# Kernel optimization log

Hardware: AMD Instinct MI355X
Metric: run time of the kernel (lower is better)

## Reference

```python
import jax, jax.numpy as jnp
import numpy as np

N = 100000
E = 1600000
D_IN = 128
HID = 128
N_CLASSES = 40
NEG_SLOPE = 0.2  # PyG GATConv default
BN_EPS = 1e-5


def setup_inputs() -> dict:
    key = jax.random.key(0)
    ks = jax.random.split(key, 16)
    s = 0.1
    return {
        "x": jax.random.normal(ks[0], (N, D_IN), dtype=jnp.float32),
        "edge_index": jax.random.randint(ks[1], (2, E), 0, N, dtype=jnp.int64),
        # GAT layer 1 (in=D_IN, out=HID, heads=1)
        "W1": jax.random.normal(ks[2], (D_IN, HID), dtype=jnp.float32) * s,
        "a_src1": jax.random.normal(ks[3], (HID,), dtype=jnp.float32) * s,
        "a_dst1": jax.random.normal(ks[4], (HID,), dtype=jnp.float32) * s,
        "b1": jnp.zeros((HID,), dtype=jnp.float32),
        # GAT layer 2 (in=HID, out=HID, heads=1)
        "W2": jax.random.normal(ks[5], (HID, HID), dtype=jnp.float32) * s,
        "a_src2": jax.random.normal(ks[6], (HID,), dtype=jnp.float32) * s,
        "a_dst2": jax.random.normal(ks[7], (HID,), dtype=jnp.float32) * s,
        "b2": jnp.zeros((HID,), dtype=jnp.float32),
        # shared BatchNorm1d(HID) applied after every conv
        "gamma": jnp.ones((HID,), dtype=jnp.float32),
        "beta": jnp.zeros((HID,), dtype=jnp.float32),
        # output Linear(HID, N_CLASSES)
        "Wout": jax.random.normal(ks[8], (HID, N_CLASSES), dtype=jnp.float32) * s,
        "bout": jnp.zeros((N_CLASSES,), dtype=jnp.float32),
    }


def reference(x, edge_index, W1, a_src1, a_dst1, b1, W2, a_src2, a_dst2, b2,
              gamma, beta, Wout, bout):
    n = x.shape[0]
    loops = jnp.arange(n, dtype=edge_index.dtype)  # add_self_loops (GATConv default)
    src = jnp.concatenate([edge_index[0], loops])
    dst = jnp.concatenate([edge_index[1], loops])

    def gat_layer(h_in, W, a_s, a_d, b):
        h = h_in @ W                                   # [N, HID]
        e_src = h @ a_s                                # [N] per-node src score
        e_dst = h @ a_d                                # [N] per-node dst score
        e = jax.nn.leaky_relu(e_src[src] + e_dst[dst], NEG_SLOPE)  # [E+N]
        # segment softmax over incoming edges of each dst node
        m = jax.ops.segment_max(e, dst, num_segments=n)
        p = jnp.exp(e - m[dst])
        denom = jax.ops.segment_sum(p, dst, num_segments=n)
        alpha = p / denom[dst]
        out = jax.ops.segment_sum(alpha[:, None] * h[src], dst, num_segments=n)
        return out + b

    def bn_elu(z):
        mu = z.mean(axis=0)
        var = ((z - mu) ** 2).mean(axis=0)  # biased var (BN training mode)
        zh = (z - mu) / jnp.sqrt(var + BN_EPS) * gamma + beta
        return jax.nn.elu(zh)

    h = bn_elu(gat_layer(x, W1, a_src1, a_dst1, b1))
    h = bn_elu(gat_layer(h, W2, a_src2, a_dst2, b2))
    return h @ Wout + bout
```

## Files before the change

kernel.cpp:

```cpp
#include <hip/hip_runtime.h>

#define NNODES 100000
#define NEDGES 1600000
#define ET (NEDGES + NNODES)
#define NBUCK 782
#define NEG 0.2f
#define BNEPS 1e-5f
#define EPB 4096
#define NBLK_E ((ET + EPB - 1) / EPB)

typedef __attribute__((ext_vector_type(8))) short short8;
typedef __attribute__((ext_vector_type(4))) float floatx4;
typedef __attribute__((ext_vector_type(2))) float floatx2;

__device__ __forceinline__ unsigned short f2b(float x) {
    unsigned int u = __float_as_uint(x);
    u += 0x7fff + ((u >> 16) & 1);
    return (unsigned short)(u >> 16);
}
__device__ __forceinline__ float b2f(unsigned short u) {
    return __uint_as_float(((unsigned int)u) << 16);
}
__device__ __forceinline__ float blo2f(unsigned int v) {
    return __uint_as_float(v << 16);
}
__device__ __forceinline__ float bhi2f(unsigned int v) {
    return __uint_as_float(v & 0xffff0000u);
}
__device__ __forceinline__ floatx2 u2f2(unsigned int v) {
    floatx2 r;
    r.x = __uint_as_float(v << 16);
    r.y = __uint_as_float(v & 0xffff0000u);
    return r;
}

__device__ __forceinline__ int edge_src(const int* ei, int e, int w64) {
    if (e >= NEDGES) return e - NEDGES;
    return w64 ? ei[2 * e] : ei[e];
}
__device__ __forceinline__ int edge_dst(const int* ei, int e, int w64) {
    if (e >= NEDGES) return e - NEDGES;
    return w64 ? ei[2 * (NEDGES + e)] : ei[NEDGES + e];
}

__global__ void k_prep(const float* __restrict__ W1, const float* __restrict__ W2,
                       unsigned short* __restrict__ WT1, unsigned short* __restrict__ WT2,
                       const int* ei, int* flag, int* bcnt, int* done, float* bnstat) {
    int t = blockIdx.x * 256 + threadIdx.x;
    if (t < 800) bcnt[t] = 0;
    if (blockIdx.x == 4) {
        bnstat[threadIdx.x] = 0.f;
    } else if (blockIdx.x == 5) {
        bnstat[256 + threadIdx.x] = 0.f;
    }
    if (t == 0) *done = 0;
    if (t == 1) {
        int is64 = 1;
        for (int j = 1; j < 16; j += 2)
            if (ei[j] != 0) is64 = 0;
        *flag = is64;
    }
    int k = t >> 7, n = t & 127;
    WT1[n * 128 + k] = f2b(W1[t]);
    WT2[n * 128 + k] = f2b(W2[t]);
}

__global__ __launch_bounds__(256) void k_bhist(const int* __restrict__ ei,
                                               const int* flag, int* bcnt,
                                               int* done, int* bbase, int* bcur) {
    __shared__ int lc[784];
    __shared__ int sh[256];
    __shared__ int lastf;
    int t = threadIdx.x;
    for (int i = t; i < NBUCK; i += 256) lc[i] = 0;
    __syncthreads();
    int w64 = *flag;
    int base = blockIdx.x * EPB;
    for (int j = 0; j < EPB / 512; j++) {
        int e = base + j * 512 + t * 2;
        if (e + 1 < NEDGES) {
            int d0, d1;
            if (w64) {
                int4 dv = *(const int4*)&ei[2 * (NEDGES + e)];
                d0 = dv.x; d1 = dv.z;
            } else {
                int2 dv = *(const int2*)&ei[NEDGES + e];
                d0 = dv.x; d1 = dv.y;
            }
            atomicAdd(&lc[d0 >> 7], 1);
            atomicAdd(&lc[d1 >> 7], 1);
        } else {
            for (int k = 0; k < 2; k++) {
                int ee = e + k;
                if (ee < ET) atomicAdd(&lc[edge_dst(ei, ee, w64) >> 7], 1);
            }
        }
    }
    __syncthreads();
    for (int i = t; i < NBUCK; i += 256)
        if (lc[i]) atomicAdd(&bcnt[i], lc[i]);
    __threadfence();
    __syncthreads();
    if (t == 0) lastf = (atomicAdd(done, 1) == gridDim.x - 1) ? 1 : 0;
    __syncthreads();
    if (!lastf) return;
    int vals[4], pre[4], sum = 0;
#pragma unroll
    for (int i = 0; i < 4; i++) {
        int id = t * 4 + i;
        int v = (id < NBUCK) ? atomicAdd(&bcnt[id], 0) : 0;
        pre[i] = sum; vals[i] = v; sum += v;
    }
    sh[t] = sum;
    __syncthreads();
    for (int off = 1; off < 256; off <<= 1) {
        int add = (t >= off) ? sh[t - off] : 0;
        __syncthreads();
        sh[t] += add;
        __syncthreads();
    }
    int excl = sh[t] - sum;
#pragma unroll
    for (int i = 0; i < 4; i++) {
        int id = t * 4 + i;
        if (id < NBUCK) { bbase[id] = excl + pre[i]; bcur[id] = excl + pre[i]; }
    }
    if (t == 255) bbase[NBUCK] = sh[255];
    (void)vals;
}

__global__ __launch_bounds__(256) void k_bscatter(const int* __restrict__ ei,
                                                  const int* flag, int* bcur,
                                                  int* __restrict__ pairs) {
    __shared__ int lc[784];
    __shared__ int lbase[784];
    int t = threadIdx.x;
    for (int i = t; i < NBUCK; i += 256) lc[i] = 0;
    __syncthreads();
    int w64 = *flag;
    int base = blockIdx.x * EPB;
    for (int j = 0; j < EPB / 512; j++) {
        int e = base + j * 512 + t * 2;
        if (e + 1 < NEDGES) {
            int d0, d1;
            if (w64) {
                int4 dv = *(const int4*)&ei[2 * (NEDGES + e)];
                d0 = dv.x; d1 = dv.z;
            } else {
                int2 dv = *(const int2*)&ei[NEDGES + e];
                d0 = dv.x; d1 = dv.y;
            }
            atomicAdd(&lc[d0 >> 7], 1);
            atomicAdd(&lc[d1 >> 7], 1);
        } else {
            for (int k = 0; k < 2; k++) {
                int ee = e + k;
                if (ee < ET) atomicAdd(&lc[edge_dst(ei, ee, w64) >> 7], 1);
            }
        }
    }
    __syncthreads();
    for (int i = t; i < NBUCK; i += 256)
        if (lc[i]) lbase[i] = atomicAdd(&bcur[i], lc[i]);
    __syncthreads();
    for (int j = 0; j < EPB / 512; j++) {
        int e = base + j * 512 + t * 2;
        if (e + 1 < NEDGES) {
            int s0, s1, d0, d1;
            if (w64) {
                int4 sv = *(const int4*)&ei[2 * e];
                int4 dv = *(const int4*)&ei[2 * (NEDGES + e)];
                s0 = sv.x; s1 = sv.z; d0 = dv.x; d1 = dv.z;
            } else {
                int2 sv = *(const int2*)&ei[e];
                int2 dv = *(const int2*)&ei[NEDGES + e];
                s0 = sv.x; s1 = sv.y; d0 = dv.x; d1 = dv.y;
            }
            int p0 = atomicAdd(&lbase[d0 >> 7], 1);
            pairs[p0] = (s0 << 7) | (d0 & 127);
            int p1 = atomicAdd(&lbase[d1 >> 7], 1);
            pairs[p1] = (s1 << 7) | (d1 & 127);
        } else {
            for (int k = 0; k < 2; k++) {
                int ee = e + k;
                if (ee < ET) {
                    int src = edge_src(ei, ee, w64);
                    int dst = edge_dst(ei, ee, w64);
                    int pos = atomicAdd(&lbase[dst >> 7], 1);
                    pairs[pos] = (src << 7) | (dst & 127);
                }
            }
        }
    }
}

__global__ __launch_bounds__(256) void k_bsort(const int* __restrict__ pairs,
                                               const int* __restrict__ bbase,
                                               int* __restrict__ rowptr,
                                               int* __restrict__ srcs) {
    __shared__ int ncnt[128];
    __shared__ int nbase[128];
    __shared__ int sscan[128];
    int b = blockIdx.x, t = threadIdx.x;
    if (t < 128) ncnt[t] = 0;
    __syncthreads();
    int s0 = bbase[b], s1 = bbase[b + 1];
    for (int i = s0 + t; i < s1; i += 256)
        atomicAdd(&ncnt[pairs[i] & 127], 1);
    __syncthreads();
    int v = (t < 128) ? ncnt[t] : 0;
    if (t < 128) sscan[t] = v;
    __syncthreads();
    for (int off = 1; off < 128; off <<= 1) {
        int add = (t < 128 && t >= off) ? sscan[t - off] : 0;
        __syncthreads();
        if (t < 128) sscan[t] += add;
        __syncthreads();
    }
    if (t < 128) {
        int excl = sscan[t] - v;
        nbase[t] = excl;
        int node = b * 128 + t;
        if (node <= NNODES) rowptr[node] = s0 + excl;
    }
    __syncthreads();
    if (t < 128) ncnt[t] = nbase[t];
    __syncthreads();
    for (int i = s0 + t; i < s1; i += 256) {
        int pr = pairs[i];
        int off = atomicAdd(&ncnt[pr & 127], 1);
        srcs[s0 + off] = ((unsigned int)pr) >> 7;
    }
}

template<bool BN>
__global__ __launch_bounds__(256) void k_gemm(const void* __restrict__ Ain,
        const unsigned short* __restrict__ WTg,
        const float* __restrict__ sums, const float* __restrict__ sqs,
        const float* __restrict__ gamma, const float* __restrict__ beta,
        const float* __restrict__ a_s, const float* __restrict__ a_d,
        float* __restrict__ es, float* __restrict__ ed,
        unsigned short* __restrict__ hB, int n) {
    __shared__ unsigned short lA[128][136];
    __shared__ unsigned short lW[128][136];
    __shared__ float las[128], lad[128];
    __shared__ float lsc[128], lsh[128];
    int t = threadIdx.x;
    int row0 = blockIdx.x * 128;
    if (t < 128) { las[t] = a_s[t]; lad[t] = a_d[t]; }
    if (BN && t < 128) {
        float mu = sums[t] * (1.f / NNODES);
        float var = fmaxf(sqs[t] * (1.f / NNODES) - mu * mu, 0.f);
        float s = gamma[t] * rsqrtf(var + BNEPS);
        lsc[t] = s;
        lsh[t] = beta[t] - mu * s;
    }

    const uint4* wt4 = (const uint4*)WTg;
#pragma unroll
    for (int j = 0; j < 8; j++) {
        int idx = t + j * 256;
        *(uint4*)&lW[idx >> 4][(idx & 15) * 8] = wt4[idx];
    }
    if (BN) __syncthreads();

    if (BN) {
        const uint4* Ab = (const uint4*)Ain;
#pragma unroll
        for (int j = 0; j < 8; j++) {
            int idx = t + j * 256;
            int r = idx >> 4, seg = idx & 15;
            uint4 v = make_uint4(0, 0, 0, 0);
            if (row0 + r < n) v = Ab[(size_t)(row0 + r) * 16 + seg];
            float f[8];
            f[0] = blo2f(v.x); f[1] = bhi2f(v.x);
            f[2] = blo2f(v.y); f[3] = bhi2f(v.y);
            f[4] = blo2f(v.z); f[5] = bhi2f(v.z);
            f[6] = blo2f(v.w); f[7] = bhi2f(v.w);
            unsigned short us[8];
#pragma unroll
            for (int k = 0; k < 8; k++) {
                int c = seg * 8 + k;
                float z = fmaf(f[k], lsc[c], lsh[c]);
                z = z > 0.f ? z : __expf(z) - 1.f;
                us[k] = f2b(z);
            }
            ushort4 u0, u1;
            u0.x = us[0]; u0.y = us[1]; u0.z = us[2]; u0.w = us[3];
            u1.x = us[4]; u1.y = us[5]; u1.z = us[6]; u1.w = us[7];
            *(ushort4*)&lA[r][seg * 8] = u0;
            *(ushort4*)&lA[r][seg * 8 + 4] = u1;
        }
    } else {
        const float* Af = (const float*)Ain;
#pragma unroll
        for (int j = 0; j < 16; j++) {
            int idx = t + j * 256;
            int r = idx >> 5, c4 = idx & 31;
            float4 v = make_float4(0.f, 0.f, 0.f, 0.f);
            if (row0 + r < n) v = ((const float4*)Af)[(size_t)(row0 + r) * 32 + c4];
            ushort4 u;
            u.x = f2b(v.x); u.y = f2b(v.y); u.z = f2b(v.z); u.w = f2b(v.w);
            *(ushort4*)&lA[r][c4 * 4] = u;
        }
    }
    __syncthreads();

    int w = t >> 6, lane = t & 63;
    int m = lane & 15, q = lane >> 4;
    int ar0 = w * 32 + m, ar1 = w * 32 + 16 + m;
    floatx4 acc0[8], acc1[8];
#pragma unroll
    for (int ct = 0; ct < 8; ct++) { acc0[ct] = (floatx4)0.0f; acc1[ct] = (floatx4)0.0f; }

#pragma unroll
    for (int kt = 0; kt < 4; kt++) {
        int kb = kt * 32 + q * 8;
        short8 af0 = *(const short8*)&lA[ar0][kb];
        short8 af1 = *(const short8*)&lA[ar1][kb];
#pragma unroll
        for (int ct = 0; ct < 8; ct++) {
            short8 bf = *(const short8*)&lW[ct * 16 + m][kb];
            acc0[ct] = __builtin_amdgcn_mfma_f32_16x16x32_bf16(af0, bf, acc0[ct], 0, 0, 0);
            acc1[ct] = __builtin_amdgcn_mfma_f32_16x16x32_bf16(af1, bf, acc1[ct], 0, 0, 0);
        }
    }

    __syncthreads();
#pragma unroll
    for (int ct = 0; ct < 8; ct++)
#pragma unroll
        for (int r = 0; r < 4; r++) {
            lA[w * 32 + q * 4 + r][ct * 16 + m] = f2b(acc0[ct][r]);
            lA[w * 32 + 16 + q * 4 + r][ct * 16 + m] = f2b(acc1[ct][r]);
        }
    __syncthreads();
#pragma unroll
    for (int j = 0; j < 8; j++) {
        int idx = t + j * 256;
        int r = idx >> 4, seg = idx & 15;
        int grow = row0 + r;
        if (grow < n) {
            uint4 v = *(const uint4*)&lA[r][seg * 8];
            ((uint4*)hB)[(size_t)grow * 16 + seg] = v;
        }
    }
    int r = t >> 1, q2 = t & 1;
    float s1 = 0.f, s2 = 0.f;
#pragma unroll
    for (int k = 0; k < 32; k++) {
        int c = q2 * 64 + 2 * k;
        unsigned int u = *(const unsigned int*)&lA[r][c];
        float va = blo2f(u), vb = bhi2f(u);
        s1 += va * las[c] + vb * las[c + 1];
        s2 += va * lad[c] + vb * lad[c + 1];
    }
    s1 += __shfl_xor(s1, 1, 64);
    s2 += __shfl_xor(s2, 1, 64);
    if (q2 == 0 && row0 + r < n) { es[row0 + r] = s1; ed[row0 + r] = s2; }
}

__global__ __launch_bounds__(256) void k_attn(const unsigned short* __restrict__ hB,
                                              const int* __restrict__ srcs,
                                              const int* __restrict__ rowptr,
                                              const float* __restrict__ es,
                                              const float* __restrict__ ed,
                                              const float* __restrict__ bias,
                                              unsigned short* __restrict__ haggB, int n) {
    __shared__ uint2 sp[8][32];
    int w = (blockIdx.x * 256 + threadIdx.x) >> 5;
    if (w >= n) return;
    int hw = threadIdx.x >> 5;
    int lane32 = threadIdx.x & 31;
    int g = lane32 >> 4, l16 = lane32 & 15;
    int start = rowptr[w], end = rowptr[w + 1];
    float edv = ed[w];
    const uint4* hp4 = (const uint4*)hB;
    floatx2 a0 = {0.f, 0.f}, a1 = {0.f, 0.f}, a2 = {0.f, 0.f}, a3 = {0.f, 0.f};
    float den = 0.f;

    for (int chunk = start; chunk < end; chunk += 32) {
        int i = chunk + lane32;
        int sv = 0; float pv = 0.f;
        if (i < end) {
            sv = srcs[i];
            float e = es[sv] + edv;
            e = e > 0.f ? e : NEG * e;
            pv = __expf(e);
            den += pv;
        }
        sp[hw][lane32] = make_uint2((unsigned)sv, __float_as_uint(pv));
        int cnt = min(32, end - chunk);
        for (int j = 0; j < cnt; j += 8) {
            uint2 e0 = sp[hw][j + g];
            uint2 e1 = sp[hw][j + 2 + g];
            uint2 e2 = sp[hw][j + 4 + g];
            uint2 e3 = sp[hw][j + 6 + g];
            uint4 h0 = hp4[e0.x * 16u + l16];
            uint4 h1 = hp4[e1.x * 16u + l16];
            uint4 h2 = hp4[e2.x * 16u + l16];
            uint4 h3 = hp4[e3.x * 16u + l16];
            float p0 = __uint_as_float(e0.y), p1 = __uint_as_float(e1.y);
            float p2 = __uint_as_float(e2.y), p3 = __uint_as_float(e3.y);
            floatx2 P0 = {p0, p0};
            a0 += P0 * u2f2(h0.x); a1 += P0 * u2f2(h0.y);
            a2 += P0 * u2f2(h0.z); a3 += P0 * u2f2(h0.w);
            floatx2 P1 = {p1, p1};
            a0 += P1 * u2f2(h1.x); a1 += P1 * u2f2(h1.y);
            a2 += P1 * u2f2(h1.z); a3 += P1 * u2f2(h1.w);
            floatx2 P2 = {p2, p2};
            a0 += P2 * u2f2(h2.x); a1 += P2 * u2f2(h2.y);
            a2 += P2 * u2f2(h2.z); a3 += P2 * u2f2(h2.w);
            floatx2 P3 = {p3, p3};
            a0 += P3 * u2f2(h3.x); a1 += P3 * u2f2(h3.y);
            a2 += P3 * u2f2(h3.z); a3 += P3 * u2f2(h3.w);
        }
    }
    den += __shfl_xor(den, 1, 64);  den += __shfl_xor(den, 2, 64);
    den += __shfl_xor(den, 4, 64);  den += __shfl_xor(den, 8, 64);
    den += __shfl_xor(den, 16, 64);
    a0.x += __shfl_xor(a0.x, 16, 64); a0.y += __shfl_xor(a0.y, 16, 64);
    a1.x += __shfl_xor(a1.x, 16, 64); a1.y += __shfl_xor(a1.y, 16, 64);
    a2.x += __shfl_xor(a2.x, 16, 64); a2.y += __shfl_xor(a2.y, 16, 64);
    a3.x += __shfl_xor(a3.x, 16, 64); a3.y += __shfl_xor(a3.y, 16, 64);
    if (g == 0) {
        float inv = 1.f / den;
        const float2* b2p = (const float2*)bias;
        float2 c0 = b2p[l16 * 4 + 0], c1 = b2p[l16 * 4 + 1];
        float2 c2 = b2p[l16 * 4 + 2], c3 = b2p[l16 * 4 + 3];
        uint4 o;
        o.x = (unsigned int)f2b(fmaf(a0.x, inv, c0.x)) |
              ((unsigned int)f2b(fmaf(a0.y, inv, c0.y)) << 16);
        o.y = (unsigned int)f2b(fmaf(a1.x, inv, c1.x)) |
              ((unsigned int)f2b(fmaf(a1.y, inv, c1.y)) << 16);
        o.z = (unsigned int)f2b(fmaf(a2.x, inv, c2.x)) |
              ((unsigned int)f2b(fmaf(a2.y, inv, c2.y)) << 16);
        o.w = (unsigned int)f2b(fmaf(a3.x, inv, c3.x)) |
              ((unsigned int)f2b(fmaf(a3.y, inv, c3.y)) << 16);
        ((uint4*)haggB)[(size_t)w * 16 + l16] = o;
    }
}

__global__ __launch_bounds__(256) void k_bnstats(const unsigned short* __restrict__ hin,
                                                 float* sums, float* sqs, int n) {
    __shared__ float red[4][256];
    int t = threadIdx.x;
    int c2 = t & 63, quarter = t >> 6;
    int r0 = blockIdx.x * 256;
    int rend = min(r0 + 256, n);
    const unsigned int* hp = (const unsigned int*)hin;
    float s0 = 0.f, q0 = 0.f, s1 = 0.f, q1 = 0.f;
    for (int r = r0 + quarter; r < rend; r += 4) {
        unsigned int v = hp[(size_t)r * 64 + c2];
        float a = blo2f(v), b = bhi2f(v);
        s0 += a; q0 += a * a;
        s1 += b; q1 += b * b;
    }
    *(float4*)&red[quarter][c2 * 4] = make_float4(s0, q0, s1, q1);
    __syncthreads();
    float v = red[0][t] + red[1][t] + red[2][t] + red[3][t];
    int c2i = t >> 2, k = t & 3;
    int ch = c2i * 2 + (k >> 1);
    if (k & 1) atomicAdd(&sqs[ch], v);
    else       atomicAdd(&sums[ch], v);
}

__global__ __launch_bounds__(256) void k_outgemm(const unsigned short* __restrict__ h,
                                                 const float* __restrict__ sums,
                                                 const float* __restrict__ sqs,
                                                 const float* __restrict__ gamma,
                                                 const float* __restrict__ beta,
                                                 const float* __restrict__ Wout,
                                                 const float* __restrict__ bout,
                                                 float* __restrict__ out, int n) {
    __shared__ float lwT[40][128];
    __shared__ float lh[64][132];
    __shared__ float lb[40];
    __shared__ float lsc[128], lsh[128];
    int t = threadIdx.x;
    if (t < 128) {
        float mu = sums[t] * (1.f / NNODES);
        float var = fmaxf(sqs[t] * (1.f / NNODES) - mu * mu, 0.f);
        float s = gamma[t] * rsqrtf(var + BNEPS);
        lsc[t] = s;
        lsh[t] = beta[t] - mu * s;
    }
    for (int idx = t; idx < 128 * 40; idx += 256) {
        int r = idx / 40, c = idx % 40;
        lwT[c][r] = Wout[idx];
    }
    if (t < 40) lb[t] = bout[t];
    __syncthreads();
    int n0 = blockIdx.x * 64;
    const uint4* hb4 = (const uint4*)h;
#pragma unroll
    for (int j = 0; j < 4; j++) {
        int idx = t + j * 256;
        int r = idx >> 4, seg = idx & 15;
        uint4 v = make_uint4(0, 0, 0, 0);
        if (n0 + r < n) v = hb4[(size_t)(n0 + r) * 16 + seg];
        float f[8];
        f[0] = blo2f(v.x); f[1] = bhi2f(v.x);
        f[2] = blo2f(v.y); f[3] = bhi2f(v.y);
        f[4] = blo2f(v.z); f[5] = bhi2f(v.z);
        f[6] = blo2f(v.w); f[7] = bhi2f(v.w);
#pragma unroll
        for (int k = 0; k < 8; k++) {
            int c = seg * 8 + k;
            float z = fmaf(f[k], lsc[c], lsh[c]);
            z = z > 0.f ? z : __expf(z) - 1.f;
            lh[r][c] = z;
        }
    }
    __syncthreads();
    int nl = t & 63, g = t >> 6;
    int row = n0 + nl;
    if (row >= n) return;
    float acc[10] = {};
    for (int k = 0; k < 128; k += 4) {
        float4 hv = *(const float4*)&lh[nl][k];
#pragma unroll
        for (int j = 0; j < 10; j++) {
            float4 wv = *(const float4*)&lwT[g * 10 + j][k];
            acc[j] += hv.x * wv.x + hv.y * wv.y + hv.z * wv.z + hv.w * wv.w;
        }
    }
#pragma unroll
    for (int j = 0; j < 10; j++)
        out[(size_t)row * 40 + g * 10 + j] = acc[j] + lb[g * 10 + j];
}

extern "C" void kernel_launch(void* const* d_in, const int* in_sizes, int n_in,
                              void* d_out, int out_size, void* d_ws, size_t ws_size,
                              hipStream_t stream) {
    const float* x      = (const float*)d_in[0];
    const int*   ei     = (const int*)d_in[1];
    const float* W1     = (const float*)d_in[2];
    const float* a_src1 = (const float*)d_in[3];
    const float* a_dst1 = (const float*)d_in[4];
    const float* b1     = (const float*)d_in[5];
    const float* W2     = (const float*)d_in[6];
    const float* a_src2 = (const float*)d_in[7];
    const float* a_dst2 = (const float*)d_in[8];
    const float* b2     = (const float*)d_in[9];
    const float* gamma  = (const float*)d_in[10];
    const float* beta   = (const float*)d_in[11];
    const float* Wout   = (const float*)d_in[12];
    const float* bout   = (const float*)d_in[13];
    float* out = (float*)d_out;

    char* p = (char*)d_ws;
    auto alloc = [&](size_t bytes) -> void* {
        void* r = (void*)p;
        p += (bytes + 255) & ~(size_t)255;
        return r;
    };
    unsigned short* hB    = (unsigned short*)alloc((size_t)NNODES * 128 * 2);
    unsigned short* haggB = (unsigned short*)alloc((size_t)NNODES * 128 * 2);
    float* es     = (float*)alloc((size_t)NNODES * 4);
    float* ed     = (float*)alloc((size_t)NNODES * 4);
    int*   pairs  = (int*)alloc((size_t)ET * 4);
    int*   srcs   = (int*)alloc((size_t)ET * 4);
    int*   rowptr = (int*)alloc((size_t)(NNODES + 1) * 4);
    int*   bcnt   = (int*)alloc(800 * 4);
    int*   bbase  = (int*)alloc(800 * 4);
    int*   bcur   = (int*)alloc(800 * 4);
    float* bnstat = (float*)alloc(4 * 128 * 4);
    unsigned short* WT1 = (unsigned short*)alloc(128 * 128 * 2);
    unsigned short* WT2 = (unsigned short*)alloc(128 * 128 * 2);
    int*   flag   = (int*)alloc(4);
    int*   done   = (int*)alloc(4);

    float* sum1 = bnstat, *sq1 = bnstat + 128, *sum2 = bnstat + 256, *sq2 = bnstat + 384;

    k_prep<<<64, 256, 0, stream>>>(W1, W2, WT1, WT2, ei, flag, bcnt, done, bnstat);
    k_bhist<<<NBLK_E, 256, 0, stream>>>(ei, flag, bcnt, done, bbase, bcur);
    k_bscatter<<<NBLK_E, 256, 0, stream>>>(ei, flag, bcur, pairs);
    k_bsort<<<NBUCK, 256, 0, stream>>>(pairs, bbase, rowptr, srcs);

    const int GB = (NNODES + 127) / 128;
    const int AB = NNODES / 8;
    const int SB = (NNODES + 255) / 256;
    const int OB = (NNODES + 63) / 64;

    k_gemm<false><<<GB, 256, 0, stream>>>(x, WT1, nullptr, nullptr, nullptr, nullptr,
                                          a_src1, a_dst1, es, ed, hB, NNODES);
    k_attn<<<AB, 256, 0, stream>>>(hB, srcs, rowptr, es, ed, b1, haggB, NNODES);
    k_bnstats<<<SB, 256, 0, stream>>>(haggB, sum1, sq1, NNODES);

    k_gemm<true><<<GB, 256, 0, stream>>>(haggB, WT2, sum1, sq1, gamma, beta,
                                         a_src2, a_dst2, es, ed, hB, NNODES);
    k_attn<<<AB, 256, 0, stream>>>(hB, srcs, rowptr, es, ed, b2, haggB, NNODES);
    k_bnstats<<<SB, 256, 0, stream>>>(haggB, sum2, sq2, NNODES);

    k_outgemm<<<OB, 256, 0, stream>>>(haggB, sum2, sq2, gamma, beta, Wout, bout, out, NNODES);

    (void)in_sizes; (void)n_in; (void)out_size; (void)ws_size;
}
```

Baseline: 446.9 us.

## Stage bucket scatter in LDS and reuse per-block histograms from k_bhist

k_bhist now writes each block's bucket histogram to global memory. k_bscatter reads that histogram instead of recounting destinations, so it no longer loads the dst indices twice. The scatter first groups pairs by bucket in shared memory and then writes them out in order, which makes the global stores more contiguous than the old random per-edge scatter. k_bnstats also drops from 256 to 64 rows per block, giving 4x more blocks but also more atomics. The cost is extra global histogram traffic and about 26KB of extra LDS per block, which may lower occupancy.

```diff
diff --git a/kernel.cpp b/kernel.cpp
--- a/kernel.cpp
+++ b/kernel.cpp
@@ -67,7 +67,8 @@
 
 __global__ __launch_bounds__(256) void k_bhist(const int* __restrict__ ei,
                                                const int* flag, int* bcnt,
-                                               int* done, int* bbase, int* bcur) {
+                                               int* done, int* bbase, int* bcur,
+                                               int* __restrict__ bh) {
     __shared__ int lc[784];
     __shared__ int sh[256];
     __shared__ int lastf;
@@ -97,19 +98,23 @@
         }
     }
     __syncthreads();
-    for (int i = t; i < NBUCK; i += 256)
-        if (lc[i]) atomicAdd(&bcnt[i], lc[i]);
+    int* bhb = bh + blockIdx.x * 784;
+    for (int i = t; i < NBUCK; i += 256) {
+        int v = lc[i];
+        bhb[i] = v;
+        if (v) atomicAdd(&bcnt[i], v);
+    }
     __threadfence();
     __syncthreads();
     if (t == 0) lastf = (atomicAdd(done, 1) == gridDim.x - 1) ? 1 : 0;
     __syncthreads();
     if (!lastf) return;
-    int vals[4], pre[4], sum = 0;
+    int pre[4], sum = 0;
 #pragma unroll
     for (int i = 0; i < 4; i++) {
         int id = t * 4 + i;
         int v = (id < NBUCK) ? atomicAdd(&bcnt[id], 0) : 0;
-        pre[i] = sum; vals[i] = v; sum += v;
+        pre[i] = sum; sum += v;
     }
     sh[t] = sum;
     __syncthreads();
@@ -126,43 +131,49 @@
         if (id < NBUCK) { bbase[id] = excl + pre[i]; bcur[id] = excl + pre[i]; }
     }
     if (t == 255) bbase[NBUCK] = sh[255];
-    (void)vals;
 }
 
 __global__ __launch_bounds__(256) void k_bscatter(const int* __restrict__ ei,
                                                   const int* flag, int* bcur,
+                                                  const int* __restrict__ bh,
                                                   int* __restrict__ pairs) {
-    __shared__ int lc[784];
+    __shared__ int lofs[784];
+    __shared__ int lcur[784];
     __shared__ int lbase[784];
+    __shared__ int sh[256];
+    __shared__ int lds_pair[4096];
+    __shared__ unsigned short lds_b[4096];
     int t = threadIdx.x;
-    for (int i = t; i < NBUCK; i += 256) lc[i] = 0;
+    const int* bhb = bh + blockIdx.x * 784;
+    int v4[4], pre4[4], sum = 0;
+#pragma unroll
+    for (int i = 0; i < 4; i++) {
+        int id = t * 4 + i;
+        int v = (id < NBUCK) ? bhb[id] : 0;
+        pre4[i] = sum; v4[i] = v; sum += v;
+    }
+    sh[t] = sum;
+    __syncthreads();
+    for (int off = 1; off < 256; off <<= 1) {
+        int add = (t >= off) ? sh[t - off] : 0;
+        __syncthreads();
+        sh[t] += add;
+        __syncthreads();
+    }
+    int excl = sh[t] - sum;
+#pragma unroll
+    for (int i = 0; i < 4; i++) {
+        int id = t * 4 + i;
+        if (id < NBUCK) {
+            int o = excl + pre4[i];
+            lofs[id] = o;
+            lcur[id] = o;
+            if (v4[i]) lbase[id] = atomicAdd(&bcur[id], v4[i]);
+        }
+    }
     __syncthreads();
     int w64 = *flag;
     int base = blockIdx.x * EPB;
-    for (int j = 0; j < EPB / 512; j++) {
-        int e = base + j * 512 + t * 2;
-        if (e + 1 < NEDGES) {
-            int d0, d1;
-            if (w64) {
-                int4 dv = *(const int4*)&ei[2 * (NEDGES + e)];
-                d0 = dv.x; d1 = dv.z;
-            } else {
-                int2 dv = *(const int2*)&ei[NEDGES + e];
-                d0 = dv.x; d1 = dv.y;
-            }
-            atomicAdd(&lc[d0 >> 7], 1);
-            atomicAdd(&lc[d1 >> 7], 1);
-        } else {
-            for (int k = 0; k < 2; k++) {
-                int ee = e + k;
-                if (ee < ET) atomicAdd(&lc[edge_dst(ei, ee, w64) >> 7], 1);
-            }
-        }
-    }
-    __syncthreads();
-    for (int i = t; i < NBUCK; i += 256)
-        if (lc[i]) lbase[i] = atomicAdd(&bcur[i], lc[i]);
-    __syncthreads();
     for (int j = 0; j < EPB / 512; j++) {
         int e = base + j * 512 + t * 2;
         if (e + 1 < NEDGES) {
@@ -176,21 +187,32 @@
                 int2 dv = *(const int2*)&ei[NEDGES + e];
                 s0 = sv.x; s1 = sv.y; d0 = dv.x; d1 = dv.y;
             }
-            int p0 = atomicAdd(&lbase[d0 >> 7], 1);
-            pairs[p0] = (s0 << 7) | (d0 & 127);
-            int p1 = atomicAdd(&lbase[d1 >> 7], 1);
-            pairs[p1] = (s1 << 7) | (d1 & 127);
+            int b0 = d0 >> 7, b1 = d1 >> 7;
+            int p0 = atomicAdd(&lcur[b0], 1);
+            lds_pair[p0] = (s0 << 7) | (d0 & 127);
+            lds_b[p0] = (unsigned short)b0;
+            int p1 = atomicAdd(&lcur[b1], 1);
+            lds_pair[p1] = (s1 << 7) | (d1 & 127);
+            lds_b[p1] = (unsigned short)b1;
         } else {
             for (int k = 0; k < 2; k++) {
                 int ee = e + k;
                 if (ee < ET) {
                     int src = edge_src(ei, ee, w64);
                     int dst = edge_dst(ei, ee, w64);
-                    int pos = atomicAdd(&lbase[dst >> 7], 1);
-                    pairs[pos] = (src << 7) | (dst & 127);
+                    int b = dst >> 7;
+                    int pos = atomicAdd(&lcur[b], 1);
+                    lds_pair[pos] = (src << 7) | (dst & 127);
+                    lds_b[pos] = (unsigned short)b;
                 }
             }
         }
+    }
+    __syncthreads();
+    int nE = ET - base; if (nE > EPB) nE = EPB;
+    for (int i = t; i < nE; i += 256) {
+        int b = lds_b[i];
+        pairs[lbase[b] + (i - lofs[b])] = lds_pair[i];
     }
 }
 
@@ -446,8 +468,8 @@
     __shared__ float red[4][256];
     int t = threadIdx.x;
     int c2 = t & 63, quarter = t >> 6;
-    int r0 = blockIdx.x * 256;
-    int rend = min(r0 + 256, n);
+    int r0 = blockIdx.x * 64;
+    int rend = min(r0 + 64, n);
     const unsigned int* hp = (const unsigned int*)hin;
     float s0 = 0.f, q0 = 0.f, s1 = 0.f, q1 = 0.f;
     for (int r = r0 + quarter; r < rend; r += 4) {
@@ -570,17 +592,18 @@
     unsigned short* WT2 = (unsigned short*)alloc(128 * 128 * 2);
     int*   flag   = (int*)alloc(4);
     int*   done   = (int*)alloc(4);
+    int*   bh     = (int*)alloc((size_t)NBLK_E * 784 * 4);
 
     float* sum1 = bnstat, *sq1 = bnstat + 128, *sum2 = bnstat + 256, *sq2 = bnstat + 384;
 
     k_prep<<<64, 256, 0, stream>>>(W1, W2, WT1, WT2, ei, flag, bcnt, done, bnstat);
-    k_bhist<<<NBLK_E, 256, 0, stream>>>(ei, flag, bcnt, done, bbase, bcur);
-    k_bscatter<<<NBLK_E, 256, 0, stream>>>(ei, flag, bcur, pairs);
+    k_bhist<<<NBLK_E, 256, 0, stream>>>(ei, flag, bcnt, done, bbase, bcur, bh);
+    k_bscatter<<<NBLK_E, 256, 0, stream>>>(ei, flag, bcur, bh, pairs);
     k_bsort<<<NBUCK, 256, 0, stream>>>(pairs, bbase, rowptr, srcs);
 
     const int GB = (NNODES + 127) / 128;
     const int AB = NNODES / 8;
-    const int SB = (NNODES + 255) / 256;
+    const int SB = (NNODES + 63) / 64;
     const int OB = (NNODES + 63) / 64;
 
     k_gemm<false><<<GB, 256, 0, stream>>>(x, WT1, nullptr, nullptr, nullptr, nullptr,
```

After: 506.8 us. 13.4% more time.
